# Optimization experiments

Hardware: AMD Instinct MI355X
Metric: run time of the kernel (lower is better)

## Reference

```python
import jax, jax.numpy as jnp
import numpy as np

N_NODES = 50000
N_EDGES = 800000
IN_CH = 128
OUT_CH = 128
N_REL = 8
N_BASES = 8


def setup_inputs() -> dict:
    key = jax.random.key(0)
    ks = jax.random.split(key, 8)
    x = jax.random.normal(ks[0], (N_NODES, IN_CH), dtype=jnp.float32)
    edge_index = jax.random.randint(ks[1], (2, N_EDGES), 0, N_NODES, dtype=jnp.int64)
    edge_type = jax.random.randint(ks[2], (N_EDGES,), 0, N_REL, dtype=jnp.int64)
    # learned parameters (PyG RGCNConv basis decomposition + root + bias, PReLU alpha)
    scale = 1.0 / np.sqrt(IN_CH)
    basis = jax.random.normal(ks[3], (N_BASES, IN_CH, OUT_CH), dtype=jnp.float32) * scale
    comp = jax.random.normal(ks[4], (N_REL, N_BASES), dtype=jnp.float32) * (1.0 / np.sqrt(N_BASES))
    root = jax.random.normal(ks[5], (IN_CH, OUT_CH), dtype=jnp.float32) * scale
    bias = jnp.zeros((OUT_CH,), dtype=jnp.float32)
    alpha = jnp.full((OUT_CH,), 0.25, dtype=jnp.float32)  # PReLU per-channel weight
    return {"x": x, "edge_index": edge_index, "edge_type": edge_type,
            "basis": basis, "comp": comp, "root": root, "bias": bias, "alpha": alpha}


def reference(x, edge_index, edge_type, basis, comp, root, bias, alpha):
    N = x.shape[0]
    R = comp.shape[0]
    # basis decomposition: W_r = sum_b comp[r,b] * basis[b]   -> [R, in, out]
    W = jnp.einsum('rb,bio->rio', comp, basis)
    # transform every node under every relation once (cheaper than per-edge matmul)
    xw = jnp.einsum('ni,rio->rno', x, W)  # [R, N, out]
    src = edge_index[0]
    dst = edge_index[1]
    msg = xw[edge_type, src]  # [E, out] gather per edge
    # PyG RGCNConv default aggr='mean': mean over incoming edges PER relation
    seg = edge_type * N + dst  # combined (relation, dst) segment id
    cnt = jax.ops.segment_sum(jnp.ones(msg.shape[0], dtype=x.dtype), seg, num_segments=R * N)
    norm = 1.0 / jnp.maximum(cnt, 1.0)
    agg = jax.ops.segment_sum(msg * norm[seg][:, None], dst, num_segments=N)  # [N, out]
    out = agg + x @ root + bias
    # PReLU with per-channel alpha
    return jnp.where(out >= 0, out, alpha * out)
```

## Files before the change

### kernel.cpp

```cpp
#include <hip/hip_runtime.h>
#include <hip/hip_bf16.h>


#define N_NODES 50000
#define N_EDGES 800000
#define N_REL   8
#define CH      128
#define KTOT    1152
#define NSEG    (N_NODES * N_REL)
#define DT      16
#define BSTRIDE 1160
#define CAP     16
#define WBLK    576
#define XBLK    6250
#define SBLK    3125
#define MAXE    448

typedef __attribute__((ext_vector_type(8))) short bf16x8;
typedef __attribute__((ext_vector_type(4))) float f32x4;

__global__ void k_prep(const float* __restrict__ basis, const float* __restrict__ comp,
                       const float* __restrict__ root, __hip_bfloat16* __restrict__ WcatT,
                       const float* __restrict__ x, unsigned int* __restrict__ xb,
                       const int* __restrict__ src, const int* __restrict__ dst,
                       const int* __restrict__ et, int* __restrict__ cnt,
                       unsigned short* __restrict__ slots) {
  int b = blockIdx.x, tid = threadIdx.x;
  if (b < WBLK) {
    int idx = b * 256 + tid;
    int o = idx / KTOT, k = idx % KTOT;
    float v;
    if (k < N_REL * CH) {
      int r = k >> 7, i = k & (CH - 1);
      float acc = 0.f;
#pragma unroll
      for (int bb = 0; bb < 8; ++bb) acc += comp[r * 8 + bb] * basis[(bb * CH + i) * CH + o];
      v = acc;
    } else {
      v = root[(k - N_REL * CH) * CH + o];
    }
    WcatT[(size_t)o * KTOT + k] = __float2bfloat16(v);
  } else if (b < WBLK + XBLK) {
    int idx = (b - WBLK) * 256 + tid;
    const float4 v = *reinterpret_cast<const float4*>(x + (size_t)idx * 4);
    __hip_bfloat16 h0 = __float2bfloat16(v.x), h1 = __float2bfloat16(v.y);
    __hip_bfloat16 h2 = __float2bfloat16(v.z), h3 = __float2bfloat16(v.w);
    xb[(size_t)idx * 2]     = *(unsigned short*)&h0 | ((unsigned int)*(unsigned short*)&h1 << 16);
    xb[(size_t)idx * 2 + 1] = *(unsigned short*)&h2 | ((unsigned int)*(unsigned short*)&h3 << 16);
  } else {
    int e = (b - WBLK - XBLK) * 256 + tid;
    int key = dst[e] * N_REL + et[e];
    int pos = atomicAdd(&cnt[key], 1);
    if (pos < CAP) slots[(size_t)key * CAP + pos] = (unsigned short)src[e];
  }
}

__global__ __launch_bounds__(512)
void k_fused(const unsigned int* __restrict__ xb, const int* __restrict__ cnt,
             const unsigned short* __restrict__ slots,
             const __hip_bfloat16* __restrict__ WcatT,
             const float* __restrict__ bias, const float* __restrict__ alpha,
             float* __restrict__ out) {
  __shared__ __hip_bfloat16 B16[DT * BSTRIDE];
  __shared__ float invc[DT * N_REL];
  __shared__ int cl[DT * N_REL];
  __shared__ int pref[DT * N_REL + 1];
  __shared__ int splits[9];
  __shared__ int elist[MAXE];
  int tid = threadIdx.x;
  int wave = tid >> 6, lane = tid & 63;
  int dstBase = blockIdx.x * DT;
  int seg0 = dstBase * N_REL;

  for (int i = tid; i < DT * 128; i += 512) {
    int row = i >> 7, c = i & 127;
    *reinterpret_cast<int4*>(&B16[row * BSTRIDE + c * 8]) = make_int4(0, 0, 0, 0);
  }
  for (int i = tid; i < DT * 64; i += 512) {
    int row = i >> 6, c = i & 63;
    *reinterpret_cast<unsigned int*>(&B16[row * BSTRIDE + 1024 + c * 2]) =
        xb[(size_t)(dstBase + row) * 64 + c];
  }
  if (tid < DT * N_REL) {
    int c = cnt[seg0 + tid];
    cl[tid] = c;
    invc[tid] = (c > 0) ? 1.0f / (float)c : 0.0f;
  }
  __syncthreads();

  if (tid < 64) {
    int a = cl[2 * tid], b2 = cl[2 * tid + 1];
    int s = a + b2, incl = s;
#pragma unroll
    for (int d = 1; d < 64; d <<= 1) {
      int t = __shfl_up(incl, d, 64);
      if (tid >= d) incl += t;
    }
    int excl = incl - s;
    pref[2 * tid] = excl;
    pref[2 * tid + 1] = excl + a;
    if (tid == 63) pref[128] = incl;
  }
  __syncthreads();

  const unsigned short* sl = slots + (size_t)seg0 * CAP;
  for (int i = tid; i < DT * N_REL * CAP; i += 512) {
    int seg = i >> 4, j = i & 15;
    if (j < cl[seg]) {
      int pos = pref[seg] + j;
      if (pos < MAXE) elist[pos] = ((int)sl[i] << 7) | seg;
    }
  }
  if (tid == 0) {
    int E = pref[128];
    splits[0] = 0; splits[8] = 128;
    int s = 0;
    for (int w = 1; w < 8; ++w) {
      int target = (w * E) >> 3;
      while (s < 128 && pref[s] < target) ++s;
      splits[w] = s;
    }
  }
  __syncthreads();

  int s0 = splits[wave], s1 = splits[wave + 1];
  int ebeg = pref[s0], eend = min(pref[s1], MAXE);
  float a0 = 0.f, a1 = 0.f;
  int curKey = -1;
  auto flush = [&]() {
    if (curKey >= 0) {
      float iv = invc[curKey];
      __hip_bfloat16 b0 = __float2bfloat16(a0 * iv);
      __hip_bfloat16 b1 = __float2bfloat16(a1 * iv);
      unsigned int pk2 = (unsigned int)*(unsigned short*)&b0 |
                         ((unsigned int)*(unsigned short*)&b1 << 16);
      *reinterpret_cast<unsigned int*>(
          &B16[(curKey >> 3) * BSTRIDE + (curKey & 7) * CH + lane * 2]) = pk2;
    }
  };
  if (ebeg < eend) {
    int l16 = lane & 15, last = eend - 1;
    int pklA = elist[min(ebeg + l16, last)];
    for (int b = ebeg; b < eend; b += 16) {
      int pk[16];
#pragma unroll
      for (int j = 0; j < 16; ++j) pk[j] = __builtin_amdgcn_readlane(pklA, j);
      unsigned u[16];
#pragma unroll
      for (int j = 0; j < 16; ++j)
        u[j] = xb[(size_t)(unsigned)(pk[j] >> 7) * 64 + lane];
      int pklB = elist[min(b + 16 + l16, last)];
#pragma unroll
      for (int j = 0; j < 16; ++j) {
        if (b + j < eend) {
          int key = pk[j] & 127;
          if (key != curKey) { flush(); curKey = key; a0 = 0.f; a1 = 0.f; }
          a0 += __uint_as_float(u[j] << 16);
          a1 += __uint_as_float(u[j] & 0xffff0000u);
        }
      }
      pklA = pklB;
    }
    flush();
  }
  __syncthreads();

  int r16 = lane & 15, g = lane >> 4;
  f32x4 acc = {0.f, 0.f, 0.f, 0.f};
  const short* Wt = reinterpret_cast<const short*>(WcatT) + (size_t)(wave * 16 + r16) * KTOT;
  const short* Arow = reinterpret_cast<const short*>(B16) + r16 * BSTRIDE;
  for (int kk = 0; kk < KTOT / 32; ++kk) {
    int kb = kk * 32 + g * 8;
    bf16x8 af = *reinterpret_cast<const bf16x8*>(Arow + kb);
    bf16x8 bw = *reinterpret_cast<const bf16x8*>(Wt + kb);
    acc = __builtin_amdgcn_mfma_f32_16x16x32_bf16(af, bw, acc, 0, 0, 0);
  }

  int col = wave * 16 + r16;
  float bi = bias[col], al = alpha[col];
#pragma unroll
  for (int rg = 0; rg < 4; ++rg) {
    int row = g * 4 + rg;
    float v = acc[rg] + bi;
    v = (v >= 0.f) ? v : al * v;
    out[(size_t)(dstBase + row) * CH + col] = v;
  }
}

extern "C" void kernel_launch(void* const* d_in, const int* in_sizes, int n_in,
                              void* d_out, int out_size, void* d_ws, size_t ws_size,
                              hipStream_t stream) {
  const float* x     = (const float*)d_in[0];
  const int*   ei    = (const int*)d_in[1];
  const int*   etype = (const int*)d_in[2];
  const float* basis = (const float*)d_in[3];
  const float* comp  = (const float*)d_in[4];
  const float* root  = (const float*)d_in[5];
  const float* bias  = (const float*)d_in[6];
  const float* alpha = (const float*)d_in[7];
  const int* src = ei;
  const int* dst = ei + N_EDGES;
  float* out = (float*)d_out;

  char* ws = (char*)d_ws;
  size_t p = 0;
  auto alloc = [&](size_t bytes) {
    void* q = ws + p;
    p = (p + bytes + 255) & ~(size_t)255;
    return q;
  };
  __hip_bfloat16* WcatT = (__hip_bfloat16*)alloc((size_t)CH * KTOT * sizeof(__hip_bfloat16));
  int* cnt  = (int*)alloc((size_t)NSEG * sizeof(int));
  unsigned short* slots = (unsigned short*)alloc((size_t)NSEG * CAP * sizeof(unsigned short));
  unsigned int* xb = (unsigned int*)alloc((size_t)N_NODES * CH / 2 * sizeof(unsigned int));

  hipMemsetAsync(cnt, 0, (size_t)NSEG * sizeof(int), stream);
  k_prep<<<WBLK + XBLK + SBLK, 256, 0, stream>>>(basis, comp, root, WcatT, x, xb,
                                                 src, dst, etype, cnt, slots);
  k_fused<<<N_NODES / DT, 512, 0, stream>>>(xb, cnt, slots, WcatT, bias, alpha, out);
}
```

Measured before the change: 230.3 us.

## Move per-block edge list compaction into a separate kernel

Compaction of the per-(dst,relation) slot lists into a packed edge list now runs in a new kernel, k_compact, which writes to a global buffer. k_fused then reads its edge list from global memory instead of building it in shared memory. This removes a scattered slot pass and one shared array from the fused kernel, which may lower its shared-memory use and improve occupancy. In exchange it adds a kernel launch and a global write and read round trip of the edge lists.

```diff
diff --git a/kernel.cpp b/kernel.cpp
--- a/kernel.cpp
+++ b/kernel.cpp
@@ -9,6 +9,7 @@
 #define KTOT    1152
 #define NSEG    (N_NODES * N_REL)
 #define DT      16
+#define NBLK    (N_NODES / DT)
 #define BSTRIDE 1160
 #define CAP     16
 #define WBLK    576
@@ -55,10 +56,42 @@
   }
 }
 
+__global__ __launch_bounds__(256)
+void k_compact(const int* __restrict__ cnt, const unsigned short* __restrict__ slots,
+               int* __restrict__ srcPkD) {
+  __shared__ int cl[128];
+  __shared__ int pref[129];
+  int b = blockIdx.x, tid = threadIdx.x;
+  int seg0 = b * 128;
+  if (tid < 128) cl[tid] = cnt[seg0 + tid];
+  __syncthreads();
+  if (tid < 64) {
+    int a = cl[2 * tid], b2 = cl[2 * tid + 1];
+    int s = a + b2, incl = s;
+#pragma unroll
+    for (int d = 1; d < 64; d <<= 1) {
+      int t = __shfl_up(incl, d, 64);
+      if (tid >= d) incl += t;
+    }
+    int excl = incl - s;
+    pref[2 * tid] = excl;
+    pref[2 * tid + 1] = excl + a;
+  }
+  __syncthreads();
+  const unsigned short* sl = slots + (size_t)seg0 * CAP;
+  int* outB = srcPkD + (size_t)b * MAXE;
+  for (int i = tid; i < 128 * CAP; i += 256) {
+    int seg = i >> 4, j = i & 15;
+    if (j < cl[seg]) {
+      int pos = pref[seg] + j;
+      if (pos < MAXE) outB[pos] = ((int)sl[i] << 7) | seg;
+    }
+  }
+}
+
 __global__ __launch_bounds__(512)
 void k_fused(const unsigned int* __restrict__ xb, const int* __restrict__ cnt,
-             const unsigned short* __restrict__ slots,
-             const __hip_bfloat16* __restrict__ WcatT,
+             const int* __restrict__ srcPkD, const __hip_bfloat16* __restrict__ WcatT,
              const float* __restrict__ bias, const float* __restrict__ alpha,
              float* __restrict__ out) {
   __shared__ __hip_bfloat16 B16[DT * BSTRIDE];
@@ -66,7 +99,6 @@
   __shared__ int cl[DT * N_REL];
   __shared__ int pref[DT * N_REL + 1];
   __shared__ int splits[9];
-  __shared__ int elist[MAXE];
   int tid = threadIdx.x;
   int wave = tid >> 6, lane = tid & 63;
   int dstBase = blockIdx.x * DT;
@@ -102,15 +134,6 @@
     if (tid == 63) pref[128] = incl;
   }
   __syncthreads();
-
-  const unsigned short* sl = slots + (size_t)seg0 * CAP;
-  for (int i = tid; i < DT * N_REL * CAP; i += 512) {
-    int seg = i >> 4, j = i & 15;
-    if (j < cl[seg]) {
-      int pos = pref[seg] + j;
-      if (pos < MAXE) elist[pos] = ((int)sl[i] << 7) | seg;
-    }
-  }
   if (tid == 0) {
     int E = pref[128];
     splits[0] = 0; splits[8] = 128;
@@ -123,6 +146,7 @@
   }
   __syncthreads();
 
+  const int* eb = srcPkD + (size_t)blockIdx.x * MAXE;
   int s0 = splits[wave], s1 = splits[wave + 1];
   int ebeg = pref[s0], eend = min(pref[s1], MAXE);
   float a0 = 0.f, a1 = 0.f;
@@ -140,7 +164,7 @@
   };
   if (ebeg < eend) {
     int l16 = lane & 15, last = eend - 1;
-    int pklA = elist[min(ebeg + l16, last)];
+    int pklA = eb[min(ebeg + l16, last)];
     for (int b = ebeg; b < eend; b += 16) {
       int pk[16];
 #pragma unroll
@@ -149,7 +173,7 @@
 #pragma unroll
       for (int j = 0; j < 16; ++j)
         u[j] = xb[(size_t)(unsigned)(pk[j] >> 7) * 64 + lane];
-      int pklB = elist[min(b + 16 + l16, last)];
+      int pklB = eb[min(b + 16 + l16, last)];
 #pragma unroll
       for (int j = 0; j < 16; ++j) {
         if (b + j < eend) {
@@ -212,10 +236,12 @@
   __hip_bfloat16* WcatT = (__hip_bfloat16*)alloc((size_t)CH * KTOT * sizeof(__hip_bfloat16));
   int* cnt  = (int*)alloc((size_t)NSEG * sizeof(int));
   unsigned short* slots = (unsigned short*)alloc((size_t)NSEG * CAP * sizeof(unsigned short));
+  int* srcPkD = (int*)alloc((size_t)NBLK * MAXE * sizeof(int));
   unsigned int* xb = (unsigned int*)alloc((size_t)N_NODES * CH / 2 * sizeof(unsigned int));
 
   hipMemsetAsync(cnt, 0, (size_t)NSEG * sizeof(int), stream);
   k_prep<<<WBLK + XBLK + SBLK, 256, 0, stream>>>(basis, comp, root, WcatT, x, xb,
                                                  src, dst, etype, cnt, slots);
-  k_fused<<<N_NODES / DT, 512, 0, stream>>>(xb, cnt, slots, WcatT, bias, alpha, out);
-}
+  k_compact<<<NBLK, 256, 0, stream>>>(cnt, slots, srcPkD);
+  k_fused<<<NBLK, 512, 0, stream>>>(xb, cnt, srcPkD, WcatT, bias, alpha, out);
+}
```

Result: faster. 223.8 us (-2.8%).
